# Optimization experiments

Measured on AMD Instinct MI355X. Metric: run time of the kernel, lower is better.

## Reference

```python
import jax, jax.numpy as jnp
import numpy as np

N_NODES = 100000
N_EDGES = 3200000
D_IN, D_HID, D_OUT = 128, 16, 2


def gcn_conv(x, src, dst, W, b, n_nodes):
    """PyG GCNConv: D^-1/2 (A+I) D^-1/2 X W + b (self-loops added, sym norm)."""
    h = x @ W  # [N, d_out] - transform before aggregation (small d_out)
    # add self loops
    loop = jnp.arange(n_nodes, dtype=src.dtype)
    src2 = jnp.concatenate([src, loop])
    dst2 = jnp.concatenate([dst, loop])
    # degree (in-degree incl. self loop) and symmetric normalization
    deg = jax.ops.segment_sum(jnp.ones_like(dst2, dtype=h.dtype), dst2,
                              num_segments=n_nodes)
    dinv = jax.lax.rsqrt(deg)  # deg >= 1 due to self loops
    norm = dinv[src2] * dinv[dst2]  # [E+N]
    msg = h[src2] * norm[:, None]   # gather + scale
    out = jax.ops.segment_sum(msg, dst2, num_segments=n_nodes)  # scatter-add
    return out + b


def setup_inputs() -> dict:
    key = jax.random.key(0)
    k1, k2, k3, k4, k5, k6 = jax.random.split(key, 6)
    x = jax.random.normal(k1, (N_NODES, D_IN), dtype=jnp.float32)
    edge_index = jax.random.randint(k2, (2, N_EDGES), 0, N_NODES, dtype=jnp.int64)
    # Glorot-style init for GCNConv weights, zero bias (PyG default)
    W1 = jax.random.normal(k3, (D_IN, D_HID), dtype=jnp.float32) / np.sqrt(D_IN)
    b1 = jnp.zeros((D_HID,), dtype=jnp.float32)
    W2 = jax.random.normal(k4, (D_HID, D_OUT), dtype=jnp.float32) / np.sqrt(D_HID)
    b2 = jnp.zeros((D_OUT,), dtype=jnp.float32)
    return {"x": x, "W1": W1, "b1": b1, "W2": W2, "b2": b2,
            "edge_index": edge_index}


def reference(x, W1, b1, W2, b2, edge_index):
    src, dst = edge_index[0], edge_index[1]
    h = jax.nn.relu(gcn_conv(x, src, dst, W1, b1, N_NODES))
    h = gcn_conv(h, src, dst, W2, b2, N_NODES)
    return jax.nn.log_softmax(h, axis=1)
```

## Files before the change

### kernel.cpp

```cpp
#include <hip/hip_runtime.h>

#define NN 100000
#define NE 3200000
#define DIN 128
#define DHID 16
#define DOUT 2
#define NBUCK 391
#define EPT 16
#define BHT 1024
#define EPB (BHT * EPT)
#define NBB ((NE + EPB - 1) / EPB)
#define P2CAP 10240

__device__ __forceinline__ unsigned f2bf(float f) {
    unsigned u = __float_as_uint(f);
    return (u + 0x7FFFu + ((u >> 16) & 1u)) >> 16;
}
__device__ __forceinline__ float bflo(unsigned a) { return __uint_as_float(a << 16); }
__device__ __forceinline__ float bfhi(unsigned a) { return __uint_as_float(a & 0xFFFF0000u); }

__global__ __launch_bounds__(512) void k_zero_b(int* __restrict__ bcount) {
    int t = threadIdx.x;
    if (t < NBUCK) bcount[t] = 0;
}

__global__ __launch_bounds__(BHT) void k_bhist(const int* __restrict__ dst,
                                               int* __restrict__ bcount) {
    __shared__ int h[NBUCK];
    int t = threadIdx.x;
    for (int i = t; i < NBUCK; i += BHT) h[i] = 0;
    __syncthreads();
    long long base = (long long)blockIdx.x * EPB;
#pragma unroll
    for (int k = 0; k < EPT; ++k) {
        long long e = base + (long long)k * BHT + t;
        if (e < NE) atomicAdd(&h[((unsigned)dst[e]) >> 8], 1);
    }
    __syncthreads();
    for (int i = t; i < NBUCK; i += BHT) {
        int c = h[i];
        if (c) atomicAdd(&bcount[i], c);
    }
}

__global__ __launch_bounds__(512) void k_bscan(const int* __restrict__ bcount,
                                               int* __restrict__ bstart,
                                               int* __restrict__ bcursor) {
    __shared__ int sc[512];
    int t = threadIdx.x;
    int c = (t < NBUCK) ? bcount[t] : 0;
    sc[t] = c;
    __syncthreads();
    for (int off = 1; off < 512; off <<= 1) {
        int v = sc[t];
        int add = (t >= off) ? sc[t - off] : 0;
        __syncthreads();
        sc[t] = v + add;
        __syncthreads();
    }
    int excl = sc[t] - c;
    if (t <= NBUCK) bstart[t] = excl;
    if (t < NBUCK) bcursor[t] = excl;
}

__global__ __launch_bounds__(BHT) void k_bfill(const int* __restrict__ src,
                                               const int* __restrict__ dst,
                                               int* __restrict__ bcursor,
                                               unsigned* __restrict__ packed) {
    __shared__ int h[NBUCK];
    __shared__ int hbase[NBUCK];
    int t = threadIdx.x;
    for (int i = t; i < NBUCK; i += BHT) h[i] = 0;
    __syncthreads();
    long long base = (long long)blockIdx.x * EPB;
    int ed[EPT], es[EPT];
#pragma unroll
    for (int k = 0; k < EPT; ++k) {
        long long e = base + (long long)k * BHT + t;
        if (e < NE) {
            ed[k] = dst[e];
            es[k] = src[e];
            atomicAdd(&h[((unsigned)ed[k]) >> 8], 1);
        } else {
            ed[k] = -1;
            es[k] = 0;
        }
    }
    __syncthreads();
    for (int i = t; i < NBUCK; i += BHT) {
        int c = h[i];
        hbase[i] = c ? atomicAdd(&bcursor[i], c) : 0;
    }
    __syncthreads();
    for (int i = t; i < NBUCK; i += BHT) h[i] = 0;
    __syncthreads();
#pragma unroll
    for (int k = 0; k < EPT; ++k) {
        if (ed[k] >= 0) {
            unsigned d = (unsigned)ed[k];
            int b = d >> 8;
            int off = atomicAdd(&h[b], 1);
            packed[hbase[b] + off] = ((d & 255u) << 24) | (unsigned)es[k];
        }
    }
}

__global__ __launch_bounds__(256) void k_pass2(const int* __restrict__ bstart,
                                               const unsigned* __restrict__ packed,
                                               int* __restrict__ rowstart,
                                               float* __restrict__ dinv,
                                               int* __restrict__ esrc) {
    __shared__ unsigned ebuf[P2CAP];
    __shared__ int h[256], sc[256], cur[256];
    int b = blockIdx.x;
    int t = threadIdx.x;
    int dst0 = b << 8;
    int ebeg = bstart[b];
    int eend = bstart[b + 1];
    int n = eend - ebeg;
    bool fits = (n <= P2CAP);
    h[t] = 0;
    __syncthreads();
    if (fits) {
        for (int i = t; i < n; i += 256) {
            unsigned pk = packed[ebeg + i];
            ebuf[i] = pk;
            atomicAdd(&h[pk >> 24], 1);
        }
    } else {
        for (int i = t; i < n; i += 256)
            atomicAdd(&h[packed[ebeg + i] >> 24], 1);
    }
    __syncthreads();
    int c = h[t];
    sc[t] = c;
    __syncthreads();
    for (int off = 1; off < 256; off <<= 1) {
        int v = sc[t];
        int add = (t >= off) ? sc[t - off] : 0;
        __syncthreads();
        sc[t] = v + add;
        __syncthreads();
    }
    int gpos = ebeg + sc[t] - c;
    int v = dst0 + t;
    if (v < NN) {
        rowstart[v] = gpos;
        dinv[v] = rsqrtf((float)(c + 1));
    }
    cur[t] = gpos;
    if (b == 0 && t == 0) rowstart[NN] = NE;
    __syncthreads();
    if (fits) {
        for (int i = t; i < n; i += 256) {
            unsigned pk = ebuf[i];
            int pos = atomicAdd(&cur[pk >> 24], 1);
            esrc[pos] = (int)(pk & 0xFFFFFFu);
        }
    } else {
        for (int i = t; i < n; i += 256) {
            unsigned pk = packed[ebeg + i];
            int pos = atomicAdd(&cur[pk >> 24], 1);
            esrc[pos] = (int)(pk & 0xFFFFFFu);
        }
    }
}

__global__ __launch_bounds__(256) void k_mm1(const float* __restrict__ x,
                                             const float* __restrict__ W1,
                                             const float* __restrict__ dinv,
                                             unsigned* __restrict__ g1b) {
    __shared__ float Ws[DIN * DHID];
    for (int i = threadIdx.x; i < DIN * DHID; i += 256) Ws[i] = W1[i];
    __syncthreads();
    int t = blockIdx.x * 256 + threadIdx.x;
    int v = t >> 2;
    int q = threadIdx.x & 3;
    if (v >= NN) return;
    float4 xq[8];
    const float4* xr = (const float4*)(x + (size_t)v * DIN + q * 32);
#pragma unroll
    for (int i = 0; i < 8; ++i) xq[i] = xr[i];
    const float* xs = (const float*)xq;
    float acc0 = 0.f, acc1 = 0.f, acc2 = 0.f, acc3 = 0.f;
#define QSTEP(QQ, CTRL)                                                          \
    _Pragma("unroll")                                                            \
    for (int k = 0; k < 32; ++k) {                                               \
        float xv = __int_as_float(                                               \
            __builtin_amdgcn_mov_dpp(__float_as_int(xs[k]), CTRL, 0xF, 0xF, false)); \
        const float4 w = *(const float4*)&Ws[(QQ * 32 + k) * DHID + q * 4];      \
        acc0 += xv * w.x; acc1 += xv * w.y; acc2 += xv * w.z; acc3 += xv * w.w;  \
    }
    QSTEP(0, 0x00)
    QSTEP(1, 0x55)
    QSTEP(2, 0xAA)
    QSTEP(3, 0xFF)
#undef QSTEP
    float dv = dinv[v];
    unsigned u0 = f2bf(acc0 * dv) | (f2bf(acc1 * dv) << 16);
    unsigned u1 = f2bf(acc2 * dv) | (f2bf(acc3 * dv) << 16);
    ((uint2*)(g1b + (size_t)v * 8))[q] = make_uint2(u0, u1);
}

__global__ __launch_bounds__(256) void k_gather1mm2(const int* __restrict__ rowstart,
                                                    const int* __restrict__ esrc,
                                                    const float* __restrict__ dinv,
                                                    const unsigned* __restrict__ G,
                                                    const float* __restrict__ b1,
                                                    const float* __restrict__ W2,
                                                    float* __restrict__ g2) {
    int t = blockIdx.x * 256 + threadIdx.x;
    int v = t >> 3;
    int j = t & 7;
    if (v >= NN) return;
    int beg = rowstart[v];
    int end = rowstart[v + 1];
    unsigned a = G[(v << 3) + j];
    float c0 = bflo(a), c1 = bfhi(a);
    int p = beg;
    int n4 = beg + ((end - beg) & ~3);
    for (; p < n4; p += 4) {
        int u0 = esrc[p], u1 = esrc[p + 1], u2 = esrc[p + 2], u3 = esrc[p + 3];
        unsigned b0 = G[(u0 << 3) + j];
        unsigned b1w = G[(u1 << 3) + j];
        unsigned b2w = G[(u2 << 3) + j];
        unsigned b3w = G[(u3 << 3) + j];
        c0 += bflo(b0) + bflo(b1w) + bflo(b2w) + bflo(b3w);
        c1 += bfhi(b0) + bfhi(b1w) + bfhi(b2w) + bfhi(b3w);
    }
    for (; p < end; ++p) {
        unsigned b = G[(esrc[p] << 3) + j];
        c0 += bflo(b);
        c1 += bfhi(b);
    }
    float dv = dinv[v];
    float o0 = fmaxf(c0 * dv + b1[2 * j], 0.f);
    float o1 = fmaxf(c1 * dv + b1[2 * j + 1], 0.f);
    float p0 = o0 * W2[(2 * j) * 2 + 0] + o1 * W2[(2 * j + 1) * 2 + 0];
    float p1 = o0 * W2[(2 * j) * 2 + 1] + o1 * W2[(2 * j + 1) * 2 + 1];
    p0 += __shfl_xor(p0, 1); p0 += __shfl_xor(p0, 2); p0 += __shfl_xor(p0, 4);
    p1 += __shfl_xor(p1, 1); p1 += __shfl_xor(p1, 2); p1 += __shfl_xor(p1, 4);
    if (j == 0) {
        float2 w = make_float2(p0 * dv, p1 * dv);
        *(float2*)(g2 + (size_t)v * 2) = w;
    }
}

__global__ __launch_bounds__(256) void k_gather2(const int* __restrict__ rowstart,
                                                 const int* __restrict__ esrc,
                                                 const float* __restrict__ dinv,
                                                 const float* __restrict__ g2,
                                                 const float* __restrict__ b2,
                                                 float* __restrict__ out) {
    int t = blockIdx.x * 256 + threadIdx.x;
    int v = t >> 3;
    if (v >= NN) return;
    int lane = t & 7;
    int ch = lane & 1;
    int slot = lane >> 1;
    int beg = rowstart[v];
    int end = rowstart[v + 1];
    float acc = 0.0f;
    for (int p = beg + slot; p < end; p += 4)
        acc += g2[(esrc[p] << 1) + ch];
    acc += __shfl_xor(acc, 2);
    acc += __shfl_xor(acc, 4);
    float o = (acc + g2[(v << 1) + ch]) * dinv[v] + b2[ch];
    float other = __shfl_xor(o, 1);
    float m = fmaxf(o, other);
    float lse = m + logf(expf(o - m) + expf(other - m));
    if (slot == 0) out[(v << 1) + ch] = o - lse;
}

extern "C" void kernel_launch(void* const* d_in, const int* in_sizes, int n_in,
                              void* d_out, int out_size, void* d_ws, size_t ws_size,
                              hipStream_t stream) {
    const float* x  = (const float*)d_in[0];
    const float* W1 = (const float*)d_in[1];
    const float* b1 = (const float*)d_in[2];
    const float* W2 = (const float*)d_in[3];
    const float* b2 = (const float*)d_in[4];
    const int* ei   = (const int*)d_in[5];
    const int* src = ei;
    const int* dst = ei + NE;

    int* ws       = (int*)d_ws;
    int* bcount   = ws;
    int* bstart   = ws + 400;
    int* bcursor  = ws + 800;
    int* rowstart = ws + 1200;
    float* dinv   = (float*)(ws + 1200 + NN + 16);
    int* esrc     = ws + 1200 + 2 * NN + 16;
    unsigned* packed = (unsigned*)(esrc + NE);
    unsigned* g1b = packed;
    float* g2     = (float*)(packed + NE);

    float* out = (float*)d_out;

    k_zero_b<<<1, 512, 0, stream>>>(bcount);
    k_bhist<<<NBB, BHT, 0, stream>>>(dst, bcount);
    k_bscan<<<1, 512, 0, stream>>>(bcount, bstart, bcursor);
    k_bfill<<<NBB, BHT, 0, stream>>>(src, dst, bcursor, packed);
    k_pass2<<<NBUCK, 256, 0, stream>>>(bstart, packed, rowstart, dinv, esrc);
    k_mm1<<<(NN * 4 + 255) / 256, 256, 0, stream>>>(x, W1, dinv, g1b);
    k_gather1mm2<<<(NN * 8 + 255) / 256, 256, 0, stream>>>(rowstart, esrc, dinv, g1b, b1, W2, g2);
    k_gather2<<<(NN * 8 + 255) / 256, 256, 0, stream>>>(rowstart, esrc, dinv, g2, b2, out);
}
```

Before: 139.3 us.

## Fuse first-layer matmul into bucket-fill kernel and apply source dinv during gather

The X·W1 transform no longer depends on dinv, so it now runs as extra blocks of the bucket-fill launch, which removes a separate kernel launch and overlaps the dense matmul with the edge scatter. To make that possible, the per-source normalisation dinv[u] is applied inside the layer-1 gather, at the cost of an extra random 4-byte load per edge. g1b moves to its own workspace region because it can no longer alias the packed buffer. The fused blocks use 1024 threads, where the old matmul kernel used 256, and they carry the Ws shared buffer, which may lower occupancy.

```diff
diff --git a/kernel.cpp b/kernel.cpp
--- a/kernel.cpp
+++ b/kernel.cpp
@@ -10,6 +10,7 @@
 #define BHT 1024
 #define EPB (BHT * EPT)
 #define NBB ((NE + EPB - 1) / EPB)
+#define MMB 391
 #define P2CAP 10240
 
 __device__ __forceinline__ unsigned f2bf(float f) {
@@ -63,13 +64,47 @@
     if (t < NBUCK) bcursor[t] = excl;
 }
 
-__global__ __launch_bounds__(BHT) void k_bfill(const int* __restrict__ src,
-                                               const int* __restrict__ dst,
-                                               int* __restrict__ bcursor,
-                                               unsigned* __restrict__ packed) {
+__global__ __launch_bounds__(BHT) void k_bfill_mm1(const int* __restrict__ src,
+                                                   const int* __restrict__ dst,
+                                                   int* __restrict__ bcursor,
+                                                   unsigned* __restrict__ packed,
+                                                   const float* __restrict__ x,
+                                                   const float* __restrict__ W1,
+                                                   unsigned* __restrict__ g1b) {
+    __shared__ float Ws[DIN * DHID];
     __shared__ int h[NBUCK];
     __shared__ int hbase[NBUCK];
     int t = threadIdx.x;
+    if (blockIdx.x >= NBB) {
+        for (int i = t; i < DIN * DHID; i += BHT) Ws[i] = W1[i];
+        __syncthreads();
+        int v = (blockIdx.x - NBB) * 256 + (t >> 2);
+        int q = t & 3;
+        if (v >= NN) return;
+        float4 xq[8];
+        const float4* xr = (const float4*)(x + (size_t)v * DIN + q * 32);
+#pragma unroll
+        for (int i = 0; i < 8; ++i) xq[i] = xr[i];
+        const float* xs = (const float*)xq;
+        float acc0 = 0.f, acc1 = 0.f, acc2 = 0.f, acc3 = 0.f;
+#define QSTEP(QQ, CTRL)                                                          \
+    _Pragma("unroll")                                                            \
+    for (int k = 0; k < 32; ++k) {                                               \
+        float xv = __int_as_float(                                               \
+            __builtin_amdgcn_mov_dpp(__float_as_int(xs[k]), CTRL, 0xF, 0xF, false)); \
+        const float4 w = *(const float4*)&Ws[(QQ * 32 + k) * DHID + q * 4];      \
+        acc0 += xv * w.x; acc1 += xv * w.y; acc2 += xv * w.z; acc3 += xv * w.w;  \
+    }
+        QSTEP(0, 0x00)
+        QSTEP(1, 0x55)
+        QSTEP(2, 0xAA)
+        QSTEP(3, 0xFF)
+#undef QSTEP
+        unsigned u0 = f2bf(acc0) | (f2bf(acc1) << 16);
+        unsigned u1 = f2bf(acc2) | (f2bf(acc3) << 16);
+        ((uint2*)(g1b + (size_t)v * 8))[q] = make_uint2(u0, u1);
+        return;
+    }
     for (int i = t; i < NBUCK; i += BHT) h[i] = 0;
     __syncthreads();
     long long base = (long long)blockIdx.x * EPB;
@@ -164,42 +199,6 @@
             esrc[pos] = (int)(pk & 0xFFFFFFu);
         }
     }
-}
-
-__global__ __launch_bounds__(256) void k_mm1(const float* __restrict__ x,
-                                             const float* __restrict__ W1,
-                                             const float* __restrict__ dinv,
-                                             unsigned* __restrict__ g1b) {
-    __shared__ float Ws[DIN * DHID];
-    for (int i = threadIdx.x; i < DIN * DHID; i += 256) Ws[i] = W1[i];
-    __syncthreads();
-    int t = blockIdx.x * 256 + threadIdx.x;
-    int v = t >> 2;
-    int q = threadIdx.x & 3;
-    if (v >= NN) return;
-    float4 xq[8];
-    const float4* xr = (const float4*)(x + (size_t)v * DIN + q * 32);
-#pragma unroll
-    for (int i = 0; i < 8; ++i) xq[i] = xr[i];
-    const float* xs = (const float*)xq;
-    float acc0 = 0.f, acc1 = 0.f, acc2 = 0.f, acc3 = 0.f;
-#define QSTEP(QQ, CTRL)                                                          \
-    _Pragma("unroll")                                                            \
-    for (int k = 0; k < 32; ++k) {                                               \
-        float xv = __int_as_float(                                               \
-            __builtin_amdgcn_mov_dpp(__float_as_int(xs[k]), CTRL, 0xF, 0xF, false)); \
-        const float4 w = *(const float4*)&Ws[(QQ * 32 + k) * DHID + q * 4];      \
-        acc0 += xv * w.x; acc1 += xv * w.y; acc2 += xv * w.z; acc3 += xv * w.w;  \
-    }
-    QSTEP(0, 0x00)
-    QSTEP(1, 0x55)
-    QSTEP(2, 0xAA)
-    QSTEP(3, 0xFF)
-#undef QSTEP
-    float dv = dinv[v];
-    unsigned u0 = f2bf(acc0 * dv) | (f2bf(acc1 * dv) << 16);
-    unsigned u1 = f2bf(acc2 * dv) | (f2bf(acc3 * dv) << 16);
-    ((uint2*)(g1b + (size_t)v * 8))[q] = make_uint2(u0, u1);
 }
 
 __global__ __launch_bounds__(256) void k_gather1mm2(const int* __restrict__ rowstart,
@@ -215,33 +214,36 @@
     if (v >= NN) return;
     int beg = rowstart[v];
     int end = rowstart[v + 1];
+    float dvv = dinv[v];
     unsigned a = G[(v << 3) + j];
-    float c0 = bflo(a), c1 = bfhi(a);
+    float c0 = dvv * bflo(a), c1 = dvv * bfhi(a);
     int p = beg;
     int n4 = beg + ((end - beg) & ~3);
     for (; p < n4; p += 4) {
         int u0 = esrc[p], u1 = esrc[p + 1], u2 = esrc[p + 2], u3 = esrc[p + 3];
+        float d0 = dinv[u0], d1 = dinv[u1], d2 = dinv[u2], d3 = dinv[u3];
         unsigned b0 = G[(u0 << 3) + j];
         unsigned b1w = G[(u1 << 3) + j];
         unsigned b2w = G[(u2 << 3) + j];
         unsigned b3w = G[(u3 << 3) + j];
-        c0 += bflo(b0) + bflo(b1w) + bflo(b2w) + bflo(b3w);
-        c1 += bfhi(b0) + bfhi(b1w) + bfhi(b2w) + bfhi(b3w);
+        c0 = fmaf(d0, bflo(b0), fmaf(d1, bflo(b1w), fmaf(d2, bflo(b2w), fmaf(d3, bflo(b3w), c0))));
+        c1 = fmaf(d0, bfhi(b0), fmaf(d1, bfhi(b1w), fmaf(d2, bfhi(b2w), fmaf(d3, bfhi(b3w), c1))));
     }
     for (; p < end; ++p) {
-        unsigned b = G[(esrc[p] << 3) + j];
-        c0 += bflo(b);
-        c1 += bfhi(b);
-    }
-    float dv = dinv[v];
-    float o0 = fmaxf(c0 * dv + b1[2 * j], 0.f);
-    float o1 = fmaxf(c1 * dv + b1[2 * j + 1], 0.f);
+        int u = esrc[p];
+        float d = dinv[u];
+        unsigned b = G[(u << 3) + j];
+        c0 = fmaf(d, bflo(b), c0);
+        c1 = fmaf(d, bfhi(b), c1);
+    }
+    float o0 = fmaxf(c0 * dvv + b1[2 * j], 0.f);
+    float o1 = fmaxf(c1 * dvv + b1[2 * j + 1], 0.f);
     float p0 = o0 * W2[(2 * j) * 2 + 0] + o1 * W2[(2 * j + 1) * 2 + 0];
     float p1 = o0 * W2[(2 * j) * 2 + 1] + o1 * W2[(2 * j + 1) * 2 + 1];
     p0 += __shfl_xor(p0, 1); p0 += __shfl_xor(p0, 2); p0 += __shfl_xor(p0, 4);
     p1 += __shfl_xor(p1, 1); p1 += __shfl_xor(p1, 2); p1 += __shfl_xor(p1, 4);
     if (j == 0) {
-        float2 w = make_float2(p0 * dv, p1 * dv);
+        float2 w = make_float2(p0 * dvv, p1 * dvv);
         *(float2*)(g2 + (size_t)v * 2) = w;
     }
 }
@@ -292,17 +294,16 @@
     float* dinv   = (float*)(ws + 1200 + NN + 16);
     int* esrc     = ws + 1200 + 2 * NN + 16;
     unsigned* packed = (unsigned*)(esrc + NE);
-    unsigned* g1b = packed;
-    float* g2     = (float*)(packed + NE);
+    unsigned* g1b = packed + NE;
+    float* g2     = (float*)(g1b + 8 * NN);
 
     float* out = (float*)d_out;
 
     k_zero_b<<<1, 512, 0, stream>>>(bcount);
     k_bhist<<<NBB, BHT, 0, stream>>>(dst, bcount);
     k_bscan<<<1, 512, 0, stream>>>(bcount, bstart, bcursor);
-    k_bfill<<<NBB, BHT, 0, stream>>>(src, dst, bcursor, packed);
+    k_bfill_mm1<<<NBB + MMB, BHT, 0, stream>>>(src, dst, bcursor, packed, x, W1, g1b);
     k_pass2<<<NBUCK, 256, 0, stream>>>(bstart, packed, rowstart, dinv, esrc);
-    k_mm1<<<(NN * 4 + 255) / 256, 256, 0, stream>>>(x, W1, dinv, g1b);
     k_gather1mm2<<<(NN * 8 + 255) / 256, 256, 0, stream>>>(rowstart, esrc, dinv, g1b, b1, W2, g2);
     k_gather2<<<(NN * 8 + 255) / 256, 256, 0, stream>>>(rowstart, esrc, dinv, g2, b2, out);
 }
```

Measured after the change: 144.2 us. +3.5%, slower.
